# Performance work log

Hardware: AMD Instinct MI355X
Metric: run time of the kernel (lower is better)

Reference implementation:

```python
import jax, jax.numpy as jnp
import numpy as np

N, K, FEAT = 64, 32, 1024      # nodes, neighbors per node, input feature dim
C1, F1 = 4, 16                 # layer1: out_channels=4, out_features=hidden[0]/4=16
C2, F2 = 32, 1                 # layer2: out_channels=hidden[1]=32, out_features=1
NUM_CLASS = 10
BN_EPS = 1e-5


def _sgnroot(x):
    return jnp.sign(x) * jnp.sqrt(jnp.clip(jnp.abs(x), 1e-8))


def _feature_adjacency(x, nb):
    # x: (N,c,f), nb: (N,K,c,f) -> adj: (N,c,f,f)
    fadj = jnp.einsum('nca,nkcb->ncab', x, nb)          # sum over K neighbors
    fadj = fadj + jnp.swapaxes(fadj, -2, -1)
    s = _sgnroot(fadj)
    out = s / (jnp.abs(s).sum(axis=1, keepdims=True) + 1e-7)  # row-normalize over channel dim
    return jnp.where(jnp.isnan(out), 0.0, out)


def _layer(x, nb, W, c_out, f_out):
    # FeatTrans1d.forward: adjacency build + batched matmul + full-width conv (== dense contraction)
    n = x.shape[0]
    adj = _feature_adjacency(x, nb)                     # (N,c,f,f)
    xa = jnp.einsum('ncab,ncb->nca', adj, x)            # adj @ x
    x2 = jnp.einsum('ocf,ncf->no', W, xa).reshape(n, c_out, f_out)
    na = jnp.einsum('ncab,nkcb->nkca', adj, nb)         # per-node adj applied to its neighbors
    nb2 = jnp.einsum('ocf,nkcf->nko', W, na).reshape(n, -1, c_out, f_out)
    return x2, nb2


def _bn_softsign_x(x, w, b):
    # BatchNorm1d (training stats over batch+feature dims) + Softsign; x: (N,C,F)
    m = x.mean(axis=(0, 2), keepdims=True)
    v = x.var(axis=(0, 2), keepdims=True)
    y = (x - m) / jnp.sqrt(v + BN_EPS) * w[None, :, None] + b[None, :, None]
    return y / (1.0 + jnp.abs(y))


def _bn_softsign_nb(x, w, b):
    # each node's neighbor set is normalized independently (list comprehension in original); x: (N,K,C,F)
    m = x.mean(axis=(1, 3), keepdims=True)
    v = x.var(axis=(1, 3), keepdims=True)
    y = (x - m) / jnp.sqrt(v + BN_EPS) * w[None, None, :, None] + b[None, None, :, None]
    return y / (1.0 + jnp.abs(y))


def setup_inputs() -> dict:
    key = jax.random.key(0)
    ks = jax.random.split(key, 6)
    return {
        'x': jax.random.normal(ks[0], (N, 1, FEAT), jnp.float32),
        'neighbor': jax.random.normal(ks[1], (N, K, 1, FEAT), jnp.float32),
        'W1': jax.random.normal(ks[2], (C1 * F1, 1, FEAT), jnp.float32) * (1.0 / FEAT) ** 0.5,
        'W2': jax.random.normal(ks[3], (C2 * F2, C1, F1), jnp.float32) * (1.0 / (C1 * F1)) ** 0.5,
        'bn1_w': jnp.ones((C1,), jnp.float32),
        'bn1_b': jnp.zeros((C1,), jnp.float32),
        'bn2_w': jnp.ones((C2,), jnp.float32),
        'bn2_b': jnp.zeros((C2,), jnp.float32),
        'lin_w': jax.random.normal(ks[4], (NUM_CLASS, C2 * F2), jnp.float32) * (1.0 / (C2 * F2)) ** 0.5,
        'lin_b': jnp.zeros((NUM_CLASS,), jnp.float32),
    }


def reference(x, neighbor, W1, W2, bn1_w, bn1_b, bn2_w, bn2_b, lin_w, lin_b):
    x1, nb1 = _layer(x, neighbor, W1, C1, F1)           # (N,4,16), (N,K,4,16)
    x1 = _bn_softsign_x(x1, bn1_w, bn1_b)
    nb1 = _bn_softsign_nb(nb1, bn1_w, bn1_b)
    x2, _ = _layer(x1, nb1, W2, C2, F2)                 # (N,32,1)
    x2 = _bn_softsign_x(x2, bn2_w, bn2_b)
    return x2.reshape(x2.shape[0], -1) @ lin_w.T + lin_b  # (N,NUM_CLASS)
```

## Files before the change

### kernel.cpp

```cpp
#include <hip/hip_runtime.h>

typedef unsigned short u16;
typedef short short8 __attribute__((ext_vector_type(8)));
typedef float floatx4 __attribute__((ext_vector_type(4)));
typedef unsigned int uintx4 __attribute__((ext_vector_type(4)));
typedef u16 ushortx4 __attribute__((ext_vector_type(4)));

#define FEAT 1024
#define KNB  32

__device__ __forceinline__ float bf2f(u16 b) { return __uint_as_float(((unsigned)b) << 16); }
__device__ __forceinline__ u16 f2bf(float f) {
    unsigned u = __float_as_uint(f);
    u += 0x7fffu + ((u >> 16) & 1u);
    return (u16)(u >> 16);
}
__device__ __forceinline__ unsigned pack2bf(float a, float b) {
    return (unsigned)f2bf(a) | ((unsigned)f2bf(b) << 16);
}

union Frag { uintx4 q; unsigned d[4]; short8 v; };

__global__ void k0_zero(float* __restrict__ pws) {
    int idx = blockIdx.x * 256 + threadIdx.x;
    if (idx < 64 * 33 * 64) pws[idx] = 0.f;
}

__global__ __launch_bounds__(256, 2) void k2_main(
    const float* __restrict__ xg, const float* __restrict__ nbg,
    const float* __restrict__ w1g, float* __restrict__ pws)
{
    __shared__ float sS[FEAT];
    __shared__ u16  sY[33 * 512];

    const int t = threadIdx.x;
    const int n = blockIdx.x >> 3;
    const int chunk = blockIdx.x & 7;
    const int chunkbase = chunk * 128;
    const int w = t >> 6;
    const int l = t & 63;
    const int m = l & 15;
    const int g = l >> 4;

    {
        const float* base = nbg + ((size_t)n * KNB) * FEAT + t * 4;
        floatx4 a = {0.f, 0.f, 0.f, 0.f};
        #pragma unroll 4
        for (int k = 0; k < KNB; ++k) {
            floatx4 qq = *(const floatx4*)(base + k * FEAT);
            a += qq;
        }
        *(floatx4*)&sS[t * 4] = a;
    }

    floatx4 acc[2][3];
    #pragma unroll
    for (int i = 0; i < 2; ++i)
        #pragma unroll
        for (int j = 0; j < 3; ++j) { floatx4 z = {0.f,0.f,0.f,0.f}; acc[i][j] = z; }

    float xa0 = xg[(size_t)n * FEAT + chunkbase + w*32 + m];
    float xa1 = xg[(size_t)n * FEAT + chunkbase + w*32 + 16 + m];
    float Sa0 = 0.f, Sa1 = 0.f;

    for (int h = 0; h < 2; ++h) {
        if (h) __syncthreads();
        for (int r = 0; r < 9; ++r) {
            int cc = t + r * 256;
            if (cc < 33 * 64) {
                int j = cc >> 6, c = cc & 63;
                const float* src = (j == 0 ? xg + (size_t)n * FEAT
                                           : nbg + ((size_t)n * KNB + (j - 1)) * FEAT)
                                   + h * 512 + c * 8;
                floatx4 f0 = *(const floatx4*)src;
                floatx4 f1 = *(const floatx4*)(src + 4);
                uintx4 vv;
                vv.x = pack2bf(f0[0], f0[1]);
                vv.y = pack2bf(f0[2], f0[3]);
                vv.z = pack2bf(f1[0], f1[1]);
                vv.w = pack2bf(f1[2], f1[3]);
                *(uintx4*)&sY[j * 512 + ((c ^ (j & 7)) * 8)] = vv;
            }
        }
        __syncthreads();
        if (h == 0) {
            Sa0 = sS[chunkbase + w*32 + m];
            Sa1 = sS[chunkbase + w*32 + 16 + m];
        }

        for (int s = 0; s < 16; ++s) {
            const int bloc = s * 32 + g * 8;
            const int c = bloc >> 3;
            Frag xbf; xbf.q = *(const uintx4*)&sY[c * 8];
            float xb[8];
            #pragma unroll
            for (int i = 0; i < 4; ++i) {
                xb[2*i]   = bf2f((u16)(xbf.d[i] & 0xffffu));
                xb[2*i+1] = bf2f((u16)(xbf.d[i] >> 16));
            }
            floatx4 sb0 = *(const floatx4*)&sS[h * 512 + bloc];
            floatx4 sb1 = *(const floatx4*)&sS[h * 512 + bloc + 4];
            float Sb[8] = {sb0[0],sb0[1],sb0[2],sb0[3],sb1[0],sb1[1],sb1[2],sb1[3]};

            Frag af0, af1;
            #pragma unroll
            for (int p = 0; p < 4; ++p) {
                float u0 = fmaf(xa0, Sb[2*p],   xb[2*p]   * Sa0);
                float u1 = fmaf(xa0, Sb[2*p+1], xb[2*p+1] * Sa0);
                af0.d[p] = 0x3F803F80u | (__float_as_uint(u1) & 0x80000000u)
                                       | ((__float_as_uint(u0) >> 16) & 0x8000u);
                float v0 = fmaf(xa1, Sb[2*p],   xb[2*p]   * Sa1);
                float v1 = fmaf(xa1, Sb[2*p+1], xb[2*p+1] * Sa1);
                af1.d[p] = 0x3F803F80u | (__float_as_uint(v1) & 0x80000000u)
                                       | ((__float_as_uint(v0) >> 16) & 0x8000u);
            }

            const int sw = (m & 7) * 8;
            Frag b0, b1, b2;
            b0.q = *(const uintx4*)&sY[ m       * 512 + ((c * 8) ^ sw)];
            b1.q = *(const uintx4*)&sY[(16 + m) * 512 + ((c * 8) ^ sw)];
            b2.q = *(const uintx4*)&sY[ 32      * 512 + c * 8];
            if (m != 0) { b2.d[0] = 0; b2.d[1] = 0; b2.d[2] = 0; b2.d[3] = 0; }

            acc[0][0] = __builtin_amdgcn_mfma_f32_16x16x32_bf16(af0.v, b0.v, acc[0][0], 0, 0, 0);
            acc[0][1] = __builtin_amdgcn_mfma_f32_16x16x32_bf16(af0.v, b1.v, acc[0][1], 0, 0, 0);
            acc[0][2] = __builtin_amdgcn_mfma_f32_16x16x32_bf16(af0.v, b2.v, acc[0][2], 0, 0, 0);
            acc[1][0] = __builtin_amdgcn_mfma_f32_16x16x32_bf16(af1.v, b0.v, acc[1][0], 0, 0, 0);
            acc[1][1] = __builtin_amdgcn_mfma_f32_16x16x32_bf16(af1.v, b1.v, acc[1][1], 0, 0, 0);
            acc[1][2] = __builtin_amdgcn_mfma_f32_16x16x32_bf16(af1.v, b2.v, acc[1][2], 0, 0, 0);
        }
    }
    __syncthreads();

    u16* sZ = sY;
    #pragma unroll
    for (int ti = 0; ti < 2; ++ti)
        #pragma unroll
        for (int jt = 0; jt < 3; ++jt) {
            int j = jt * 16 + m;
            int aloc = w * 32 + ti * 16 + g * 4;
            ushortx4 zz;
            zz.x = f2bf(acc[ti][jt][0]);
            zz.y = f2bf(acc[ti][jt][1]);
            zz.z = f2bf(acc[ti][jt][2]);
            zz.w = f2bf(acc[ti][jt][3]);
            *(ushortx4*)&sZ[j * 136 + aloc] = zz;
        }
    __syncthreads();

    floatx4 a2[3];
    #pragma unroll
    for (int j = 0; j < 3; ++j) { floatx4 z = {0.f,0.f,0.f,0.f}; a2[j] = z; }
    #pragma unroll
    for (int kc = 0; kc < 4; ++kc) {
        const float* wsrc = w1g + (size_t)(w * 16 + m) * FEAT + chunkbase + kc * 32 + g * 8;
        floatx4 wf0 = *(const floatx4*)wsrc;
        floatx4 wf1 = *(const floatx4*)(wsrc + 4);
        Frag wb;
        wb.d[0] = pack2bf(wf0[0], wf0[1]);
        wb.d[1] = pack2bf(wf0[2], wf0[3]);
        wb.d[2] = pack2bf(wf1[0], wf1[1]);
        wb.d[3] = pack2bf(wf1[2], wf1[3]);
        #pragma unroll
        for (int jt = 0; jt < 3; ++jt) {
            Frag za;
            za.q = *(const uintx4*)&sZ[(jt * 16 + m) * 136 + kc * 32 + g * 8];
            a2[jt] = __builtin_amdgcn_mfma_f32_16x16x32_bf16(za.v, wb.v, a2[jt], 0, 0, 0);
        }
    }
    float* pbase = pws + (size_t)n * 33 * 64;
    #pragma unroll
    for (int jt = 0; jt < 3; ++jt)
        #pragma unroll
        for (int r = 0; r < 4; ++r) {
            int j = jt * 16 + g * 4 + r;
            if (j < 33) atomicAdd(&pbase[j * 64 + w * 16 + m], a2[jt][r]);
        }
}

__global__ __launch_bounds__(256) void k3_bnx(
    const float* __restrict__ pws, const float* __restrict__ bn1w,
    const float* __restrict__ bn1b, float* __restrict__ x1ws)
{
    __shared__ float sx2[64 * 64];
    __shared__ float ssc[4], sbi[4];
    const int t = threadIdx.x;
    #pragma unroll
    for (int r = 0; r < 16; ++r) {
        int idx = t + r * 256;
        int nn = idx >> 6, o = idx & 63;
        sx2[idx] = pws[(size_t)nn * 2112 + o];
    }
    __syncthreads();
    {
        int cc = t >> 6, l2 = t & 63;
        float s = 0.f, s2 = 0.f;
        #pragma unroll
        for (int i = 0; i < 16; ++i) {
            int idx = l2 * 16 + i;
            int nn = idx >> 4, f = idx & 15;
            float v = sx2[nn * 64 + cc * 16 + f];
            s += v; s2 += v * v;
        }
        #pragma unroll
        for (int off = 32; off > 0; off >>= 1) {
            s  += __shfl_down(s, off);
            s2 += __shfl_down(s2, off);
        }
        if (l2 == 0) {
            float mean = s * (1.f / 1024.f);
            float var = s2 * (1.f / 1024.f) - mean * mean;
            float rs = rsqrtf(var + 1e-5f);
            float wv = bn1w[cc], bv = bn1b[cc];
            ssc[cc] = rs * wv;
            sbi[cc] = bv - mean * rs * wv;
        }
    }
    __syncthreads();
    #pragma unroll
    for (int r = 0; r < 16; ++r) {
        int idx = t + r * 256;
        int o = idx & 63, cc = o >> 4;
        float v = sx2[idx] * ssc[cc] + sbi[cc];
        x1ws[idx] = v / (1.f + fabsf(v));
    }
}

__global__ __launch_bounds__(256) void k3_node(
    const float* __restrict__ pws, const float* __restrict__ x1ws,
    const float* __restrict__ bn1w, const float* __restrict__ bn1b,
    const float* __restrict__ w2g, float* __restrict__ x22ws)
{
    __shared__ float snb[32 * 64];
    __shared__ float sx1[64], sS1[64], sadj[4 * 16 * 16], sxa[64];
    __shared__ float ssc[4], sbi[4];
    const int t = threadIdx.x;
    const int n = blockIdx.x;

    #pragma unroll
    for (int r = 0; r < 8; ++r) {
        int idx = t + r * 256;
        int k = idx >> 6, o = idx & 63;
        snb[idx] = pws[(size_t)n * 2112 + (1 + k) * 64 + o];
    }
    if (t < 64) sx1[t] = x1ws[n * 64 + t];
    __syncthreads();
    {
        int cc = t >> 6, l2 = t & 63;
        float s = 0.f, s2 = 0.f;
        #pragma unroll
        for (int i = 0; i < 8; ++i) {
            int idx = l2 * 8 + i;
            int k = idx >> 4, f = idx & 15;
            float v = snb[k * 64 + cc * 16 + f];
            s += v; s2 += v * v;
        }
        #pragma unroll
        for (int off = 32; off > 0; off >>= 1) {
            s  += __shfl_down(s, off);
            s2 += __shfl_down(s2, off);
        }
        if (l2 == 0) {
            float mean = s * (1.f / 512.f);
            float var = s2 * (1.f / 512.f) - mean * mean;
            float rs = rsqrtf(var + 1e-5f);
            float wv = bn1w[cc], bv = bn1b[cc];
            ssc[cc] = rs * wv;
            sbi[cc] = bv - mean * rs * wv;
        }
    }
    __syncthreads();
    if (t < 64) {
        int cc = t >> 4;
        float a = 0.f;
        for (int k = 0; k < 32; ++k) {
            float v = snb[k * 64 + t] * ssc[cc] + sbi[cc];
            a += v / (1.f + fabsf(v));
        }
        sS1[t] = a;
    }
    __syncthreads();
    {
        int a = t >> 4, b = t & 15;
        float sc[4]; float den = 1e-7f;
        #pragma unroll
        for (int c = 0; c < 4; ++c) {
            float u = sx1[c * 16 + a] * sS1[c * 16 + b] + sx1[c * 16 + b] * sS1[c * 16 + a];
            float r = sqrtf(fmaxf(fabsf(u), 1e-8f));
            sc[c] = copysignf(r, u);
            den += r;
        }
        float inv = 1.f / den;
        #pragma unroll
        for (int c = 0; c < 4; ++c) sadj[(c * 16 + a) * 16 + b] = sc[c] * inv;
    }
    __syncthreads();
    if (t < 64) {
        int cc = t >> 4;
        float a = 0.f;
        #pragma unroll
        for (int b = 0; b < 16; ++b) a += sadj[t * 16 + b] * sx1[cc * 16 + b];
        sxa[t] = a;
    }
    __syncthreads();
    if (t < 32) {
        float a = 0.f;
        #pragma unroll
        for (int cf = 0; cf < 64; ++cf) a += w2g[t * 64 + cf] * sxa[cf];
        x22ws[n * 32 + t] = a;
    }
}

__global__ __launch_bounds__(256) void k3_fin(
    const float* __restrict__ x22ws, const float* __restrict__ bn2w,
    const float* __restrict__ bn2b, const float* __restrict__ linw,
    const float* __restrict__ linb, float* __restrict__ outg)
{
    __shared__ float sx[64 * 32];
    __shared__ float sy[64 * 32];
    __shared__ float ssc[32], sbi[32];
    const int t = threadIdx.x;
    #pragma unroll
    for (int r = 0; r < 8; ++r) sx[t + r * 256] = x22ws[t + r * 256];
    __syncthreads();
    if (t < 32) {
        float s = 0.f, s2 = 0.f;
        for (int nn = 0; nn < 64; ++nn) {
            float v = sx[nn * 32 + t];
            s += v; s2 += v * v;
        }
        float mean = s * (1.f / 64.f);
        float var = s2 * (1.f / 64.f) - mean * mean;
        float rs = rsqrtf(var + 1e-5f);
        float wv = bn2w[t], bv = bn2b[t];
        ssc[t] = rs * wv;
        sbi[t] = bv - mean * rs * wv;
    }
    __syncthreads();
    #pragma unroll
    for (int r = 0; r < 8; ++r) {
        int idx = t + r * 256;
        int o = idx & 31;
        float v = sx[idx] * ssc[o] + sbi[o];
        sy[idx] = v / (1.f + fabsf(v));
    }
    __syncthreads();
    for (int r = 0; r < 3; ++r) {
        int idx = t + r * 256;
        if (idx < 640) {
            int nn = idx / 10, cls = idx % 10;
            float a = linb[cls];
            #pragma unroll
            for (int o = 0; o < 32; ++o) a += sy[nn * 32 + o] * linw[cls * 32 + o];
            outg[idx] = a;
        }
    }
}

extern "C" void kernel_launch(void* const* d_in, const int* in_sizes, int n_in,
                              void* d_out, int out_size, void* d_ws, size_t ws_size,
                              hipStream_t stream) {
    (void)in_sizes; (void)n_in; (void)out_size; (void)ws_size;
    const float* xg   = (const float*)d_in[0];
    const float* nbg  = (const float*)d_in[1];
    const float* w1g  = (const float*)d_in[2];
    const float* w2g  = (const float*)d_in[3];
    const float* bn1w = (const float*)d_in[4];
    const float* bn1b = (const float*)d_in[5];
    const float* bn2w = (const float*)d_in[6];
    const float* bn2b = (const float*)d_in[7];
    const float* linw = (const float*)d_in[8];
    const float* linb = (const float*)d_in[9];

    float* pws   = (float*)d_ws;
    float* x1ws  = pws + (size_t)64 * 33 * 64;
    float* x22ws = x1ws + 64 * 64;
    float* outg  = (float*)d_out;

    k0_zero<<<dim3(528), dim3(256), 0, stream>>>(pws);
    k2_main<<<dim3(512), dim3(256), 0, stream>>>(xg, nbg, w1g, pws);
    k3_bnx<<<dim3(1), dim3(256), 0, stream>>>(pws, bn1w, bn1b, x1ws);
    k3_node<<<dim3(64), dim3(256), 0, stream>>>(pws, x1ws, bn1w, bn1b, w2g, x22ws);
    k3_fin<<<dim3(1), dim3(256), 0, stream>>>(x22ws, bn2w, bn2b, linw, linb, outg);
}
```

Measured before the change: 118.7 us.

## Drop zero kernel and atomics, fuse BN stages, stage full rows once

The main kernel now stages the whole 1024-wide x and neighbor rows into shared memory as bf16 in a single pass, fused with the neighbor sum. The two half passes and their extra barrier are gone. Per-chunk partials are written with plain stores to separate slots instead of atomics, so the zero-init kernel can be removed. The batch-norm stats kernel and the per-node kernel are merged into one 64-block kernel that reduces the 8 chunk partials and recomputes the global x statistics in every block. Launches drop from five to three, at the cost of more shared memory per block (which may limit occupancy) and redundant global-stat work in each block.

```diff
diff --git a/kernel.cpp b/kernel.cpp
--- a/kernel.cpp
+++ b/kernel.cpp
@@ -3,13 +3,14 @@
 typedef unsigned short u16;
 typedef short short8 __attribute__((ext_vector_type(8)));
 typedef float floatx4 __attribute__((ext_vector_type(4)));
+typedef float floatx2 __attribute__((ext_vector_type(2)));
 typedef unsigned int uintx4 __attribute__((ext_vector_type(4)));
+typedef unsigned int uintx2 __attribute__((ext_vector_type(2)));
 typedef u16 ushortx4 __attribute__((ext_vector_type(4)));
 
 #define FEAT 1024
 #define KNB  32
 
-__device__ __forceinline__ float bf2f(u16 b) { return __uint_as_float(((unsigned)b) << 16); }
 __device__ __forceinline__ u16 f2bf(float f) {
     unsigned u = __float_as_uint(f);
     u += 0x7fffu + ((u >> 16) & 1u);
@@ -18,20 +19,17 @@
 __device__ __forceinline__ unsigned pack2bf(float a, float b) {
     return (unsigned)f2bf(a) | ((unsigned)f2bf(b) << 16);
 }
+__device__ __forceinline__ float softsign(float v) { return v / (1.f + fabsf(v)); }
 
 union Frag { uintx4 q; unsigned d[4]; short8 v; };
-
-__global__ void k0_zero(float* __restrict__ pws) {
-    int idx = blockIdx.x * 256 + threadIdx.x;
-    if (idx < 64 * 33 * 64) pws[idx] = 0.f;
-}
 
 __global__ __launch_bounds__(256, 2) void k2_main(
     const float* __restrict__ xg, const float* __restrict__ nbg,
     const float* __restrict__ w1g, float* __restrict__ pws)
 {
     __shared__ float sS[FEAT];
-    __shared__ u16  sY[33 * 512];
+    __shared__ float sX[FEAT];
+    __shared__ u16  sY[34 * 1024];
 
     const int t = threadIdx.x;
     const int n = blockIdx.x >> 3;
@@ -43,92 +41,84 @@
     const int g = l >> 4;
 
     {
-        const float* base = nbg + ((size_t)n * KNB) * FEAT + t * 4;
-        floatx4 a = {0.f, 0.f, 0.f, 0.f};
+        ushortx4 z4 = {0, 0, 0, 0};
+        *(ushortx4*)&sY[33 * 1024 + t * 4] = z4;
+    }
+    {
+        floatx4 xv = *(const floatx4*)(xg + (size_t)n * FEAT + t * 4);
+        *(floatx4*)&sX[t * 4] = xv;
+        ushortx4 xb4 = {f2bf(xv[0]), f2bf(xv[1]), f2bf(xv[2]), f2bf(xv[3])};
+        *(ushortx4*)&sY[t * 4] = xb4;
+    }
+    {
+        const float* nbase = nbg + ((size_t)n * KNB) * FEAT + t * 4;
+        floatx4 sacc = {0.f, 0.f, 0.f, 0.f};
         #pragma unroll 4
         for (int k = 0; k < KNB; ++k) {
-            floatx4 qq = *(const floatx4*)(base + k * FEAT);
-            a += qq;
-        }
-        *(floatx4*)&sS[t * 4] = a;
-    }
+            floatx4 v = *(const floatx4*)(nbase + (size_t)k * FEAT);
+            sacc += v;
+            int row = k + 1;
+            int c16 = (t >> 1) ^ (row & 7);
+            ushortx4 p4 = {f2bf(v[0]), f2bf(v[1]), f2bf(v[2]), f2bf(v[3])};
+            *(ushortx4*)&sY[row * 1024 + c16 * 8 + (t & 1) * 4] = p4;
+        }
+        *(floatx4*)&sS[t * 4] = sacc;
+    }
+
+    const float xa0 = xg[(size_t)n * FEAT + chunkbase + w * 32 + m];
+    const float xa1 = xg[(size_t)n * FEAT + chunkbase + w * 32 + 16 + m];
+    __syncthreads();
+    const float Sa0 = sS[chunkbase + w * 32 + m];
+    const float Sa1 = sS[chunkbase + w * 32 + 16 + m];
+
+    const u16* b2base = (m == 0) ? &sY[32 * 1024] : &sY[33 * 1024];
+    const int sw = (m & 7);
 
     floatx4 acc[2][3];
     #pragma unroll
     for (int i = 0; i < 2; ++i)
         #pragma unroll
-        for (int j = 0; j < 3; ++j) { floatx4 z = {0.f,0.f,0.f,0.f}; acc[i][j] = z; }
-
-    float xa0 = xg[(size_t)n * FEAT + chunkbase + w*32 + m];
-    float xa1 = xg[(size_t)n * FEAT + chunkbase + w*32 + 16 + m];
-    float Sa0 = 0.f, Sa1 = 0.f;
-
-    for (int h = 0; h < 2; ++h) {
-        if (h) __syncthreads();
-        for (int r = 0; r < 9; ++r) {
-            int cc = t + r * 256;
-            if (cc < 33 * 64) {
-                int j = cc >> 6, c = cc & 63;
-                const float* src = (j == 0 ? xg + (size_t)n * FEAT
-                                           : nbg + ((size_t)n * KNB + (j - 1)) * FEAT)
-                                   + h * 512 + c * 8;
-                floatx4 f0 = *(const floatx4*)src;
-                floatx4 f1 = *(const floatx4*)(src + 4);
-                uintx4 vv;
-                vv.x = pack2bf(f0[0], f0[1]);
-                vv.y = pack2bf(f0[2], f0[3]);
-                vv.z = pack2bf(f1[0], f1[1]);
-                vv.w = pack2bf(f1[2], f1[3]);
-                *(uintx4*)&sY[j * 512 + ((c ^ (j & 7)) * 8)] = vv;
-            }
-        }
-        __syncthreads();
-        if (h == 0) {
-            Sa0 = sS[chunkbase + w*32 + m];
-            Sa1 = sS[chunkbase + w*32 + 16 + m];
-        }
-
-        for (int s = 0; s < 16; ++s) {
-            const int bloc = s * 32 + g * 8;
-            const int c = bloc >> 3;
-            Frag xbf; xbf.q = *(const uintx4*)&sY[c * 8];
-            float xb[8];
-            #pragma unroll
-            for (int i = 0; i < 4; ++i) {
-                xb[2*i]   = bf2f((u16)(xbf.d[i] & 0xffffu));
-                xb[2*i+1] = bf2f((u16)(xbf.d[i] >> 16));
-            }
-            floatx4 sb0 = *(const floatx4*)&sS[h * 512 + bloc];
-            floatx4 sb1 = *(const floatx4*)&sS[h * 512 + bloc + 4];
-            float Sb[8] = {sb0[0],sb0[1],sb0[2],sb0[3],sb1[0],sb1[1],sb1[2],sb1[3]};
-
-            Frag af0, af1;
-            #pragma unroll
-            for (int p = 0; p < 4; ++p) {
-                float u0 = fmaf(xa0, Sb[2*p],   xb[2*p]   * Sa0);
-                float u1 = fmaf(xa0, Sb[2*p+1], xb[2*p+1] * Sa0);
-                af0.d[p] = 0x3F803F80u | (__float_as_uint(u1) & 0x80000000u)
-                                       | ((__float_as_uint(u0) >> 16) & 0x8000u);
-                float v0 = fmaf(xa1, Sb[2*p],   xb[2*p]   * Sa1);
-                float v1 = fmaf(xa1, Sb[2*p+1], xb[2*p+1] * Sa1);
-                af1.d[p] = 0x3F803F80u | (__float_as_uint(v1) & 0x80000000u)
-                                       | ((__float_as_uint(v0) >> 16) & 0x8000u);
-            }
-
-            const int sw = (m & 7) * 8;
-            Frag b0, b1, b2;
-            b0.q = *(const uintx4*)&sY[ m       * 512 + ((c * 8) ^ sw)];
-            b1.q = *(const uintx4*)&sY[(16 + m) * 512 + ((c * 8) ^ sw)];
-            b2.q = *(const uintx4*)&sY[ 32      * 512 + c * 8];
-            if (m != 0) { b2.d[0] = 0; b2.d[1] = 0; b2.d[2] = 0; b2.d[3] = 0; }
-
-            acc[0][0] = __builtin_amdgcn_mfma_f32_16x16x32_bf16(af0.v, b0.v, acc[0][0], 0, 0, 0);
-            acc[0][1] = __builtin_amdgcn_mfma_f32_16x16x32_bf16(af0.v, b1.v, acc[0][1], 0, 0, 0);
-            acc[0][2] = __builtin_amdgcn_mfma_f32_16x16x32_bf16(af0.v, b2.v, acc[0][2], 0, 0, 0);
-            acc[1][0] = __builtin_amdgcn_mfma_f32_16x16x32_bf16(af1.v, b0.v, acc[1][0], 0, 0, 0);
-            acc[1][1] = __builtin_amdgcn_mfma_f32_16x16x32_bf16(af1.v, b1.v, acc[1][1], 0, 0, 0);
-            acc[1][2] = __builtin_amdgcn_mfma_f32_16x16x32_bf16(af1.v, b2.v, acc[1][2], 0, 0, 0);
-        }
+        for (int j = 0; j < 3; ++j) { floatx4 z = {0.f, 0.f, 0.f, 0.f}; acc[i][j] = z; }
+
+    const floatx2 vxa0 = {xa0, xa0}, vxa1 = {xa1, xa1};
+    const floatx2 vSa0 = {Sa0, Sa0}, vSa1 = {Sa1, Sa1};
+
+    #pragma unroll 2
+    for (int s = 0; s < 32; ++s) {
+        const int bloc = s * 32 + g * 8;
+        const int cidx = bloc >> 3;
+
+        floatx4 xq0 = *(const floatx4*)&sX[bloc];
+        floatx4 xq1 = *(const floatx4*)&sX[bloc + 4];
+        floatx4 sq0 = *(const floatx4*)&sS[bloc];
+        floatx4 sq1 = *(const floatx4*)&sS[bloc + 4];
+
+        Frag af0, af1;
+        #pragma unroll
+        for (int p = 0; p < 4; ++p) {
+            floatx2 xbp = (p < 2) ? ((p == 0) ? (floatx2){xq0[0], xq0[1]} : (floatx2){xq0[2], xq0[3]})
+                                  : ((p == 2) ? (floatx2){xq1[0], xq1[1]} : (floatx2){xq1[2], xq1[3]});
+            floatx2 sbp = (p < 2) ? ((p == 0) ? (floatx2){sq0[0], sq0[1]} : (floatx2){sq0[2], sq0[3]})
+                                  : ((p == 2) ? (floatx2){sq1[0], sq1[1]} : (floatx2){sq1[2], sq1[3]});
+            floatx2 u0 = xbp * vSa0 + sbp * vxa0;
+            floatx2 u1 = xbp * vSa1 + sbp * vxa1;
+            uintx2 b0b = __builtin_bit_cast(uintx2, u0);
+            uintx2 b1b = __builtin_bit_cast(uintx2, u1);
+            af0.d[p] = 0x3F803F80u | (b0b.y & 0x80000000u) | ((b0b.x >> 16) & 0x8000u);
+            af1.d[p] = 0x3F803F80u | (b1b.y & 0x80000000u) | ((b1b.x >> 16) & 0x8000u);
+        }
+
+        Frag b0, b1, b2;
+        b0.q = *(const uintx4*)&sY[ m       * 1024 + ((cidx ^ sw) << 3)];
+        b1.q = *(const uintx4*)&sY[(16 + m) * 1024 + ((cidx ^ sw) << 3)];
+        b2.q = *(const uintx4*)&b2base[cidx << 3];
+
+        acc[0][0] = __builtin_amdgcn_mfma_f32_16x16x32_bf16(af0.v, b0.v, acc[0][0], 0, 0, 0);
+        acc[0][1] = __builtin_amdgcn_mfma_f32_16x16x32_bf16(af0.v, b1.v, acc[0][1], 0, 0, 0);
+        acc[0][2] = __builtin_amdgcn_mfma_f32_16x16x32_bf16(af0.v, b2.v, acc[0][2], 0, 0, 0);
+        acc[1][0] = __builtin_amdgcn_mfma_f32_16x16x32_bf16(af1.v, b0.v, acc[1][0], 0, 0, 0);
+        acc[1][1] = __builtin_amdgcn_mfma_f32_16x16x32_bf16(af1.v, b1.v, acc[1][1], 0, 0, 0);
+        acc[1][2] = __builtin_amdgcn_mfma_f32_16x16x32_bf16(af1.v, b2.v, acc[1][2], 0, 0, 0);
     }
     __syncthreads();
 
@@ -150,7 +140,7 @@
 
     floatx4 a2[3];
     #pragma unroll
-    for (int j = 0; j < 3; ++j) { floatx4 z = {0.f,0.f,0.f,0.f}; a2[j] = z; }
+    for (int j = 0; j < 3; ++j) { floatx4 z = {0.f, 0.f, 0.f, 0.f}; a2[j] = z; }
     #pragma unroll
     for (int kc = 0; kc < 4; ++kc) {
         const float* wsrc = w1g + (size_t)(w * 16 + m) * FEAT + chunkbase + kc * 32 + g * 8;
@@ -168,28 +158,45 @@
             a2[jt] = __builtin_amdgcn_mfma_f32_16x16x32_bf16(za.v, wb.v, a2[jt], 0, 0, 0);
         }
     }
-    float* pbase = pws + (size_t)n * 33 * 64;
+    float* pbase = pws + (size_t)(n * 8 + chunk) * 33 * 64;
     #pragma unroll
     for (int jt = 0; jt < 3; ++jt)
         #pragma unroll
         for (int r = 0; r < 4; ++r) {
             int j = jt * 16 + g * 4 + r;
-            if (j < 33) atomicAdd(&pbase[j * 64 + w * 16 + m], a2[jt][r]);
-        }
-}
-
-__global__ __launch_bounds__(256) void k3_bnx(
+            if (j < 33) pbase[j * 64 + w * 16 + m] = a2[jt][r];
+        }
+}
+
+__global__ __launch_bounds__(256) void kB(
     const float* __restrict__ pws, const float* __restrict__ bn1w,
-    const float* __restrict__ bn1b, float* __restrict__ x1ws)
+    const float* __restrict__ bn1b, const float* __restrict__ w2g,
+    float* __restrict__ x22ws)
 {
     __shared__ float sx2[64 * 64];
-    __shared__ float ssc[4], sbi[4];
+    __shared__ float snb[32 * 64];
+    __shared__ float sx1[64], sS1[64], sadj[4 * 16 * 16], sxa[64];
+    __shared__ float ssc[4], sbi[4], ssc2[4], sbi2[4];
     const int t = threadIdx.x;
+    const int n = blockIdx.x;
+
     #pragma unroll
     for (int r = 0; r < 16; ++r) {
         int idx = t + r * 256;
         int nn = idx >> 6, o = idx & 63;
-        sx2[idx] = pws[(size_t)nn * 2112 + o];
+        float v = 0.f;
+        #pragma unroll
+        for (int c = 0; c < 8; ++c) v += pws[(size_t)((nn * 8 + c) * 33) * 64 + o];
+        sx2[idx] = v;
+    }
+    #pragma unroll
+    for (int r = 0; r < 8; ++r) {
+        int idx = t + r * 256;
+        int k = idx >> 6, o = idx & 63;
+        float v = 0.f;
+        #pragma unroll
+        for (int c = 0; c < 8; ++c) v += pws[(size_t)((n * 8 + c) * 33 + 1 + k) * 64 + o];
+        snb[idx] = v;
     }
     __syncthreads();
     {
@@ -202,81 +209,40 @@
             float v = sx2[nn * 64 + cc * 16 + f];
             s += v; s2 += v * v;
         }
-        #pragma unroll
-        for (int off = 32; off > 0; off >>= 1) {
-            s  += __shfl_down(s, off);
-            s2 += __shfl_down(s2, off);
-        }
-        if (l2 == 0) {
-            float mean = s * (1.f / 1024.f);
-            float var = s2 * (1.f / 1024.f) - mean * mean;
-            float rs = rsqrtf(var + 1e-5f);
-            float wv = bn1w[cc], bv = bn1b[cc];
-            ssc[cc] = rs * wv;
-            sbi[cc] = bv - mean * rs * wv;
-        }
-    }
-    __syncthreads();
-    #pragma unroll
-    for (int r = 0; r < 16; ++r) {
-        int idx = t + r * 256;
-        int o = idx & 63, cc = o >> 4;
-        float v = sx2[idx] * ssc[cc] + sbi[cc];
-        x1ws[idx] = v / (1.f + fabsf(v));
-    }
-}
-
-__global__ __launch_bounds__(256) void k3_node(
-    const float* __restrict__ pws, const float* __restrict__ x1ws,
-    const float* __restrict__ bn1w, const float* __restrict__ bn1b,
-    const float* __restrict__ w2g, float* __restrict__ x22ws)
-{
-    __shared__ float snb[32 * 64];
-    __shared__ float sx1[64], sS1[64], sadj[4 * 16 * 16], sxa[64];
-    __shared__ float ssc[4], sbi[4];
-    const int t = threadIdx.x;
-    const int n = blockIdx.x;
-
-    #pragma unroll
-    for (int r = 0; r < 8; ++r) {
-        int idx = t + r * 256;
-        int k = idx >> 6, o = idx & 63;
-        snb[idx] = pws[(size_t)n * 2112 + (1 + k) * 64 + o];
-    }
-    if (t < 64) sx1[t] = x1ws[n * 64 + t];
-    __syncthreads();
-    {
-        int cc = t >> 6, l2 = t & 63;
-        float s = 0.f, s2 = 0.f;
+        float s3 = 0.f, s4 = 0.f;
         #pragma unroll
         for (int i = 0; i < 8; ++i) {
             int idx = l2 * 8 + i;
             int k = idx >> 4, f = idx & 15;
             float v = snb[k * 64 + cc * 16 + f];
-            s += v; s2 += v * v;
+            s3 += v; s4 += v * v;
         }
         #pragma unroll
         for (int off = 32; off > 0; off >>= 1) {
-            s  += __shfl_down(s, off);
-            s2 += __shfl_down(s2, off);
+            s  += __shfl_down(s, off);  s2 += __shfl_down(s2, off);
+            s3 += __shfl_down(s3, off); s4 += __shfl_down(s4, off);
         }
         if (l2 == 0) {
-            float mean = s * (1.f / 512.f);
-            float var = s2 * (1.f / 512.f) - mean * mean;
+            float wv = bn1w[cc], bv = bn1b[cc];
+            float mean = s * (1.f / 1024.f);
+            float var = s2 * (1.f / 1024.f) - mean * mean;
             float rs = rsqrtf(var + 1e-5f);
-            float wv = bn1w[cc], bv = bn1b[cc];
             ssc[cc] = rs * wv;
             sbi[cc] = bv - mean * rs * wv;
+            float mean2 = s3 * (1.f / 512.f);
+            float var2 = s4 * (1.f / 512.f) - mean2 * mean2;
+            float rs2 = rsqrtf(var2 + 1e-5f);
+            ssc2[cc] = rs2 * wv;
+            sbi2[cc] = bv - mean2 * rs2 * wv;
         }
     }
     __syncthreads();
     if (t < 64) {
         int cc = t >> 4;
+        sx1[t] = softsign(sx2[n * 64 + t] * ssc[cc] + sbi[cc]);
         float a = 0.f;
-        for (int k = 0; k < 32; ++k) {
-            float v = snb[k * 64 + t] * ssc[cc] + sbi[cc];
-            a += v / (1.f + fabsf(v));
-        }
+        for (int k = 0; k < KNB; ++k)
+            a += softsign(snb[k * 64 + t] * ssc2[cc] + sbi2[cc]);
         sS1[t] = a;
     }
     __syncthreads();
@@ -311,14 +277,14 @@
     }
 }
 
-__global__ __launch_bounds__(256) void k3_fin(
+__global__ __launch_bounds__(256) void kC(
     const float* __restrict__ x22ws, const float* __restrict__ bn2w,
     const float* __restrict__ bn2b, const float* __restrict__ linw,
     const float* __restrict__ linb, float* __restrict__ outg)
 {
-    __shared__ float sx[64 * 32];
     __shared__ float sy[64 * 32];
     __shared__ float ssc[32], sbi[32];
+    __shared__ float sx[64 * 32];
     const int t = threadIdx.x;
     #pragma unroll
     for (int r = 0; r < 8; ++r) sx[t + r * 256] = x22ws[t + r * 256];
@@ -341,8 +307,7 @@
     for (int r = 0; r < 8; ++r) {
         int idx = t + r * 256;
         int o = idx & 31;
-        float v = sx[idx] * ssc[o] + sbi[o];
-        sy[idx] = v / (1.f + fabsf(v));
+        sy[idx] = softsign(sx[idx] * ssc[o] + sbi[o]);
     }
     __syncthreads();
     for (int r = 0; r < 3; ++r) {
@@ -373,13 +338,10 @@
     const float* linb = (const float*)d_in[9];
 
     float* pws   = (float*)d_ws;
-    float* x1ws  = pws + (size_t)64 * 33 * 64;
-    float* x22ws = x1ws + 64 * 64;
+    float* x22ws = pws + (size_t)64 * 8 * 33 * 64;
     float* outg  = (float*)d_out;
 
-    k0_zero<<<dim3(528), dim3(256), 0, stream>>>(pws);
     k2_main<<<dim3(512), dim3(256), 0, stream>>>(xg, nbg, w1g, pws);
-    k3_bnx<<<dim3(1), dim3(256), 0, stream>>>(pws, bn1w, bn1b, x1ws);
-    k3_node<<<dim3(64), dim3(256), 0, stream>>>(pws, x1ws, bn1w, bn1b, w2g, x22ws);
-    k3_fin<<<dim3(1), dim3(256), 0, stream>>>(x22ws, bn2w, bn2b, linw, linb, outg);
-}
+    kB<<<dim3(64), dim3(256), 0, stream>>>(pws, bn1w, bn1b, w2g, x22ws);
+    kC<<<dim3(1), dim3(256), 0, stream>>>(x22ws, bn2w, bn2b, linw, linb, outg);
+}
```

After: 140.9 us. +18.6%, slower.
